# Kernel optimization log

Hardware: AMD Instinct MI355X
Metric: run time of the kernel (lower is better)

Reference implementation:

```python
import jax, jax.numpy as jnp
import numpy as np

B, T, C, E, H, K = 4, 2048, 1024, 8, 2048, 2


def setup_inputs() -> dict:
    key = jax.random.key(0)
    k1, k2, k3, k4 = jax.random.split(key, 4)
    x = jax.random.normal(k1, (B, T, C), jnp.float32)
    router_w = jax.random.normal(k2, (E, C), jnp.float32) * 0.02
    fc_w = jax.random.normal(k3, (E, H, C), jnp.float32) * 0.02
    proj_w = jax.random.normal(k4, (E, C, H), jnp.float32) * 0.02
    return {"x": x, "router_w": router_w, "fc_w": fc_w, "proj_w": proj_w}


def reference(x, router_w, fc_w, proj_w):
    Bb, Tt, Cc = x.shape
    Ee = router_w.shape[0]
    k = K
    N = Bb * Tt
    x_flat = x.reshape(N, Cc)

    # Router: linear -> softmax -> top-k, renormalize
    scores = x_flat @ router_w.T                       # [N, E]
    routing_weights = jax.nn.softmax(scores, axis=-1)  # [N, E]
    top_w, top_idx = jax.lax.top_k(routing_weights, k) # [N, k]
    top_w = top_w / (top_w.sum(-1, keepdims=True) + 1e-10)

    flat_expert_ids = top_idx.reshape(-1)              # [N*k]
    flat_weights = top_w.reshape(-1)
    flat_token_ids = jnp.repeat(jnp.arange(N), k)

    # Stable sort by expert id (token permute)
    order = jnp.argsort(flat_expert_ids, stable=True)
    se = flat_expert_ids[order]
    st = flat_token_ids[order]
    sw = flat_weights[order]
    permuted_x = x_flat[st]                            # [N*k, C]

    tokens_per_expert = jnp.bincount(flat_expert_ids, length=Ee)
    offsets = jnp.concatenate([jnp.zeros((1,), tokens_per_expert.dtype),
                               jnp.cumsum(tokens_per_expert)[:-1]])
    pos_in_expert = jnp.arange(N * k) - offsets[se]
    capacity = 2 * N * k // Ee
    flat_batch_idx = se * capacity + pos_in_expert
    valid = pos_in_expert < capacity

    # Scatter tokens into capacity-padded per-expert batches (overflow dropped)
    scatter_idx = jnp.where(valid, flat_batch_idx, Ee * capacity)  # OOB => drop
    batched_x = jnp.zeros((Ee * capacity, Cc), x.dtype).at[scatter_idx].set(
        permuted_x, mode='drop')
    batched_x = batched_x.reshape(Ee, capacity, Cc)

    # Grouped GEMM: fc -> relu^2 -> proj
    hidden = jnp.square(jax.nn.relu(jnp.einsum('eic,ehc->eih', batched_x, fc_w)))
    batched_out = jnp.einsum('eih,ech->eic', hidden, proj_w).reshape(Ee * capacity, Cc)

    # Gather back, weight, scatter-add combine
    gathered = batched_out[jnp.where(valid, flat_batch_idx, 0)]
    weighted = gathered * jnp.where(valid, sw, 0.0)[:, None]
    output = jnp.zeros((N, Cc), x.dtype).at[st].add(weighted)
    return output.reshape(Bb, Tt, Cc), routing_weights.reshape(Bb, Tt, Ee)
```

## Files before the change

### kernel.cpp

```cpp
#include <hip/hip_runtime.h>
#include <hip/hip_bf16.h>
#include <stdint.h>

#define NB 4
#define NTT 2048
#define NC 1024
#define NE 8
#define NH 2048
#define NKK 2
#define NTOK (NB * NTT)
#define CAP (2 * NTOK * NKK / NE)

typedef __hip_bfloat16 bf16;
typedef __attribute__((ext_vector_type(8))) short short8;
typedef __attribute__((ext_vector_type(4))) short short4v;
typedef __attribute__((ext_vector_type(4))) float floatx4;
typedef __attribute__((ext_vector_type(2))) float floatx2;

typedef const __attribute__((address_space(1))) void* gas_ptr;
typedef __attribute__((address_space(3))) void* las_ptr;

static __device__ __forceinline__ void async_copy16(const void* g, void* l) {
  __builtin_amdgcn_global_load_lds((gas_ptr)g, (las_ptr)l, 16, 0, 0);
}

static __device__ __forceinline__ unsigned short f2b(float f) {
  bf16 h = __float2bfloat16(f);
  unsigned short u;
  __builtin_memcpy(&u, &h, 2);
  return u;
}
static __device__ __forceinline__ int iclamp(int v, int lo, int hi) {
  return v < lo ? lo : (v > hi ? hi : v);
}

__global__ __launch_bounds__(256) void zero_out_kernel(float* __restrict__ out) {
  const size_t i = ((size_t)blockIdx.x * 256 + threadIdx.x) * 4;
  floatx4 z = {0.f, 0.f, 0.f, 0.f};
  *reinterpret_cast<floatx4*>(out + i) = z;
}

__global__ __launch_bounds__(256) void cvt_kernel(const float* __restrict__ src,
                                                  bf16* __restrict__ dst) {
  const size_t i = ((size_t)blockIdx.x * 256 + threadIdx.x) * 8;
  const floatx4 a = *reinterpret_cast<const floatx4*>(src + i);
  const floatx4 b = *reinterpret_cast<const floatx4*>(src + i + 4);
  short8 r;
  r[0] = (short)f2b(a[0]); r[1] = (short)f2b(a[1]);
  r[2] = (short)f2b(a[2]); r[3] = (short)f2b(a[3]);
  r[4] = (short)f2b(b[0]); r[5] = (short)f2b(b[1]);
  r[6] = (short)f2b(b[2]); r[7] = (short)f2b(b[3]);
  *reinterpret_cast<short8*>(dst + i) = r;
}

__global__ __launch_bounds__(256) void router_kernel(
    const float* __restrict__ x, const float* __restrict__ rw,
    float* __restrict__ rw_out, int* __restrict__ epair,
    float* __restrict__ wpair, bf16* __restrict__ xb) {
  __shared__ float rws[NE * NC];
  const int tid = threadIdx.x;
  {
    const floatx4* rw4 = reinterpret_cast<const floatx4*>(rw);
    floatx4* rwl4 = reinterpret_cast<floatx4*>(rws);
#pragma unroll
    for (int i = 0; i < 8; ++i) rwl4[i * 256 + tid] = rw4[i * 256 + tid];
  }
  __syncthreads();

  const int wave = tid >> 6;
  const int lane = tid & 63;
  const int t = blockIdx.x * 4 + wave;
  const floatx4* xr4 = reinterpret_cast<const floatx4*>(x + (size_t)t * NC);
  const floatx4* rwl4 = reinterpret_cast<const floatx4*>(rws);
  bf16* xbr = xb + (size_t)t * NC;

  floatx4 xv[4];
#pragma unroll
  for (int i = 0; i < 4; ++i) xv[i] = xr4[i * 64 + lane];

#pragma unroll
  for (int i = 0; i < 4; ++i) {
    const int idx = i * 64 + lane;
    short4v o;
    o[0] = (short)f2b(xv[i][0]); o[1] = (short)f2b(xv[i][1]);
    o[2] = (short)f2b(xv[i][2]); o[3] = (short)f2b(xv[i][3]);
    *reinterpret_cast<short4v*>(xbr + idx * 4) = o;
  }

  float acc[NE];
#pragma unroll
  for (int e = 0; e < NE; ++e) acc[e] = 0.f;
#pragma unroll
  for (int i = 0; i < 4; ++i) {
    const int idx = i * 64 + lane;
#pragma unroll
    for (int e = 0; e < NE; ++e) {
      const floatx4 wv = rwl4[e * 256 + idx];
      acc[e] = fmaf(xv[i][0], wv[0], acc[e]);
      acc[e] = fmaf(xv[i][1], wv[1], acc[e]);
      acc[e] = fmaf(xv[i][2], wv[2], acc[e]);
      acc[e] = fmaf(xv[i][3], wv[3], acc[e]);
    }
  }
#pragma unroll
  for (int e = 0; e < NE; ++e) {
#pragma unroll
    for (int off = 32; off; off >>= 1) acc[e] += __shfl_xor(acc[e], off, 64);
  }

  float m = acc[0];
#pragma unroll
  for (int e = 1; e < NE; ++e) m = fmaxf(m, acc[e]);
  float p[NE];
  float s = 0.f;
#pragma unroll
  for (int e = 0; e < NE; ++e) {
    p[e] = __expf(acc[e] - m);
    s += p[e];
  }
  const float inv = 1.f / s;
#pragma unroll
  for (int e = 0; e < NE; ++e) p[e] *= inv;

  if (lane < NE) rw_out[(size_t)t * NE + lane] = p[lane];

  if (lane == 0) {
    int i0 = 0;
    float v0 = p[0];
    int i1 = -1;
    float v1 = -1.f;
#pragma unroll
    for (int e = 1; e < NE; ++e) {
      if (p[e] > v0) {
        v1 = v0; i1 = i0;
        v0 = p[e]; i0 = e;
      } else if (p[e] > v1) {
        v1 = p[e]; i1 = e;
      }
    }
    i0 = iclamp(i0, 0, NE - 1);
    i1 = iclamp(i1, 0, NE - 1);
    const float denom = v0 + v1 + 1e-10f;
    epair[t] = i0 | (i1 << 16);
    floatx2 wv;
    wv[0] = v0 / denom;
    wv[1] = v1 / denom;
    *reinterpret_cast<floatx2*>(wpair + 2 * t) = wv;
  }
}

__global__ __launch_bounds__(256) void build_kernel(
    const int* __restrict__ epair, const float* __restrict__ wpair,
    int* __restrict__ cnt, int* __restrict__ tok, float* __restrict__ wslot) {
  const int e = blockIdx.x;
  const int tid = threadIdx.x;
  const int lane = tid & 63;
  const int wave = tid >> 6;
  constexpr int TPT = NTOK / 256;
  const int t0 = tid * TPT;

  int pe[TPT];
#pragma unroll
  for (int i = 0; i < TPT; i += 4) {
    const int4 v = *reinterpret_cast<const int4*>(epair + t0 + i);
    pe[i] = v.x; pe[i + 1] = v.y; pe[i + 2] = v.z; pe[i + 3] = v.w;
  }
  int c = 0;
#pragma unroll
  for (int i = 0; i < TPT; ++i)
    c += (((pe[i] & 0xffff) == e) ? 1 : 0) + (((pe[i] >> 16) == e) ? 1 : 0);

  int incl = c;
#pragma unroll
  for (int off = 1; off < 64; off <<= 1) {
    const int up = __shfl_up(incl, off, 64);
    if (lane >= off) incl += up;
  }
  __shared__ int wsum[4];
  if (lane == 63) wsum[wave] = incl;
  __syncthreads();
  int base = incl - c;
#pragma unroll
  for (int w = 0; w < 4; ++w)
    if (w < wave) base += wsum[w];
  if (tid == 255) cnt[e] = base + c;

#pragma unroll
  for (int i = 0; i < TPT; ++i) {
    const int t = t0 + i;
    if ((pe[i] & 0xffff) == e) {
      if (base < CAP) {
        tok[e * CAP + base] = t;
        wslot[e * CAP + base] = wpair[2 * t];
      }
      ++base;
    }
    if ((pe[i] >> 16) == e) {
      if (base < CAP) {
        tok[e * CAP + base] = t;
        wslot[e * CAP + base] = wpair[2 * t + 1];
      }
      ++base;
    }
  }
}

template <bool FC>
__global__ __launch_bounds__(256) void gemm_moe(
    const bf16* __restrict__ Axb, const bf16* __restrict__ Ah,
    const bf16* __restrict__ Bw, bf16* __restrict__ Oh,
    float* __restrict__ Oo, const int* __restrict__ cnt,
    const int* __restrict__ tok, const float* __restrict__ wslot,
    int rowOffset, int mch) {
  constexpr int Kd = FC ? NC : NH;
  constexpr int Nd = FC ? NH : NC;
  const int e = blockIdx.z;
  const int Me = iclamp(cnt[e], 0, CAP);
  const int rowBase = rowOffset + blockIdx.y * 128;
  if (rowBase >= Me) return;
  const int colBase = blockIdx.x * 128;

  const bf16* __restrict__ Be = Bw + (size_t)e * Nd * Kd;
  const bf16* __restrict__ Ahc = Ah + (size_t)e * mch * NH;

  __shared__ bf16 As[128 * 64];
  __shared__ bf16 Bs[128 * 64];

  const int tid = threadIdx.x;
  const int lane = tid & 63;
  const int wid = tid >> 6;
  const int wm = wid & 1;
  const int wn = wid >> 1;
  const int ml = lane & 15;
  const int quad = lane >> 4;

  const bf16* ga[4];
  const bf16* gb[4];
  bf16* la[4];
  bf16* lb[4];
#pragma unroll
  for (int it = 0; it < 4; ++it) {
    const int sidx = it * 256 + tid;
    const int r = sidx >> 3;
    const int pc = sidx & 7;
    const int lc = pc ^ (r & 7);
    if (FC) {
      const int grow = rowBase + r;
      const int tk = (grow < Me) ? tok[e * CAP + grow] : 0;
      const int arow = iclamp(tk, 0, NTOK - 1);
      ga[it] = Axb + (size_t)arow * NC + lc * 8;
    } else {
      int grow = rowBase + r;
      if (grow > Me - 1) grow = Me - 1;
      const int arow = iclamp(grow - rowOffset, 0, mch - 1);
      ga[it] = Ahc + (size_t)arow * NH + lc * 8;
    }
    gb[it] = Be + (size_t)(colBase + r) * Kd + lc * 8;
    la[it] = As + sidx * 8;
    lb[it] = Bs + sidx * 8;
  }

  floatx4 acc[4][4];
#pragma unroll
  for (int mt = 0; mt < 4; ++mt)
#pragma unroll
    for (int nt = 0; nt < 4; ++nt) acc[mt][nt] = floatx4{0.f, 0.f, 0.f, 0.f};

  int aoff[4][2], boff[4][2];
#pragma unroll
  for (int t4 = 0; t4 < 4; ++t4)
#pragma unroll
    for (int kk = 0; kk < 2; ++kk) {
      const int ra = wm * 64 + t4 * 16 + ml;
      const int rb = wn * 64 + t4 * 16 + ml;
      const int q = kk * 4 + quad;
      aoff[t4][kk] = (ra * 8 + (q ^ (ra & 7))) * 8;
      boff[t4][kk] = (rb * 8 + (q ^ (rb & 7))) * 8;
    }

#pragma unroll
  for (int it = 0; it < 4; ++it) async_copy16(ga[it], la[it]);
#pragma unroll
  for (int it = 0; it < 4; ++it) async_copy16(gb[it], lb[it]);

  const int nkb = Kd >> 6;
  for (int kb = 0; kb < nkb; ++kb) {
    __syncthreads();
    short8 af[4][2], bff[4][2];
#pragma unroll
    for (int mt = 0; mt < 4; ++mt)
#pragma unroll
      for (int kk = 0; kk < 2; ++kk)
        af[mt][kk] = *reinterpret_cast<const short8*>(&As[aoff[mt][kk]]);
#pragma unroll
    for (int nt = 0; nt < 4; ++nt)
#pragma unroll
      for (int kk = 0; kk < 2; ++kk)
        bff[nt][kk] = *reinterpret_cast<const short8*>(&Bs[boff[nt][kk]]);
#pragma unroll
    for (int kk = 0; kk < 2; ++kk)
#pragma unroll
      for (int mt = 0; mt < 4; ++mt)
#pragma unroll
        for (int nt = 0; nt < 4; ++nt)
          acc[mt][nt] = __builtin_amdgcn_mfma_f32_16x16x32_bf16(
              af[mt][kk], bff[nt][kk], acc[mt][nt], 0, 0, 0);
    __syncthreads();
    if (kb + 1 < nkb) {
      const int k0 = (kb + 1) << 6;
#pragma unroll
      for (int it = 0; it < 4; ++it) async_copy16(ga[it] + k0, la[it]);
#pragma unroll
      for (int it = 0; it < 4; ++it) async_copy16(gb[it] + k0, lb[it]);
    }
  }

  if (FC) {
    bf16* __restrict__ O = Oh + (size_t)e * mch * NH;
    const int rlBase = rowBase - rowOffset;
#pragma unroll
    for (int mt = 0; mt < 4; ++mt) {
      const int rl = wm * 64 + mt * 16 + quad * 4;
#pragma unroll
      for (int nt = 0; nt < 4; ++nt) {
        const int cc = colBase + wn * 64 + nt * 16 + ml;
        const floatx4 v = acc[mt][nt];
#pragma unroll
        for (int rg = 0; rg < 4; ++rg) {
          if (rowBase + rl + rg < Me) {
            float f = fmaxf(v[rg], 0.f);
            f = f * f;
            O[(size_t)(rlBase + rl + rg) * NH + cc] = __float2bfloat16(f);
          }
        }
      }
    }
  } else {
#pragma unroll
    for (int mt = 0; mt < 4; ++mt) {
      const int rl = wm * 64 + mt * 16 + quad * 4;
#pragma unroll
      for (int rg = 0; rg < 4; ++rg) {
        const int re = rowBase + rl + rg;
        if (re < Me) {
          const int t = iclamp(tok[e * CAP + re], 0, NTOK - 1);
          const float w = wslot[e * CAP + re];
#pragma unroll
          for (int nt = 0; nt < 4; ++nt) {
            const int cc = colBase + wn * 64 + nt * 16 + ml;
            atomicAdd(Oo + (size_t)t * NC + cc, w * acc[mt][nt][rg]);
          }
        }
      }
    }
  }
}

extern "C" void kernel_launch(void* const* d_in, const int* in_sizes, int n_in,
                              void* d_out, int out_size, void* d_ws,
                              size_t ws_size, hipStream_t stream) {
  const float* x = (const float*)d_in[0];
  const float* rw = (const float*)d_in[1];
  const float* fcw = (const float*)d_in[2];
  const float* pjw = (const float*)d_in[3];
  float* out = (float*)d_out;
  float* rw_out = out + (size_t)NTOK * NC;

  char* ws = (char*)d_ws;
  int* cnt = (int*)ws;
  int* tok = (int*)(ws + 256);
  float* wslot = (float*)(ws + 256 + 131072);
  int* epair = (int*)(ws + 262400);
  float* wpair = (float*)(ws + 262400 + 32768);
  bf16* xb = (bf16*)(ws + 360704);
  bf16* fcwb = (bf16*)(ws + 360704 + 16777216);
  bf16* pjwb = (bf16*)(ws + 360704 + 16777216 + 33554432);
  const size_t fixed = 360704 + 16777216 + 2 * 33554432;
  bf16* hidden = (bf16*)(ws + fixed);
  (void)in_sizes; (void)n_in; (void)out_size;

  int mch = 128;
  for (int cand = CAP; cand >= 128; cand >>= 1) {
    const size_t need = fixed + (size_t)NE * cand * NH * 2;
    if (need <= ws_size) { mch = cand; break; }
  }

  zero_out_kernel<<<NTOK * NC / 1024, 256, 0, stream>>>(out);
  cvt_kernel<<<NE * NH * NC / 2048, 256, 0, stream>>>(fcw, fcwb);
  cvt_kernel<<<NE * NC * NH / 2048, 256, 0, stream>>>(pjw, pjwb);
  router_kernel<<<NTOK / 4, 256, 0, stream>>>(x, rw, rw_out, epair, wpair, xb);
  build_kernel<<<NE, 256, 0, stream>>>(epair, wpair, cnt, tok, wslot);

  for (int c = 0; c < CAP / mch; ++c) {
    gemm_moe<true><<<dim3(NH / 128, mch / 128, NE), 256, 0, stream>>>(
        xb, hidden, fcwb, hidden, out, cnt, tok, wslot, c * mch, mch);
    gemm_moe<false><<<dim3(NC / 128, mch / 128, NE), 256, 0, stream>>>(
        xb, hidden, pjwb, hidden, out, cnt, tok, wslot, c * mch, mch);
  }
}
```

Measured before the change: 475.0 us.

## Use 256x256 tiles, 512 threads and double-buffered LDS pipeline in MoE GEMM

The grouped GEMM block tile grows from 128x128 to 256x256 with 512 threads and 8x4 MFMA tiles per wave. The K loop becomes a double-buffered LDS pipeline: the next slice is prefetched with explicit vmcnt waits and raw barriers, and MFMA sections get raised priority. The aim is more operand reuse per load and global-to-LDS copies hidden behind compute. In exchange LDS use rises to 128 KB per block and register pressure is higher, which may limit occupancy. Partially filled expert tiles also waste more work because tile granularity is coarser.

```diff
diff --git a/kernel.cpp b/kernel.cpp
--- a/kernel.cpp
+++ b/kernel.cpp
@@ -206,7 +206,7 @@
 }
 
 template <bool FC>
-__global__ __launch_bounds__(256) void gemm_moe(
+__global__ __launch_bounds__(512, 2) void gemm_moe(
     const bf16* __restrict__ Axb, const bf16* __restrict__ Ah,
     const bf16* __restrict__ Bw, bf16* __restrict__ Oh,
     float* __restrict__ Oo, const int* __restrict__ cnt,
@@ -216,15 +216,15 @@
   constexpr int Nd = FC ? NH : NC;
   const int e = blockIdx.z;
   const int Me = iclamp(cnt[e], 0, CAP);
-  const int rowBase = rowOffset + blockIdx.y * 128;
+  const int rowBase = rowOffset + blockIdx.y * 256;
   if (rowBase >= Me) return;
-  const int colBase = blockIdx.x * 128;
+  const int colBase = blockIdx.x * 256;
 
   const bf16* __restrict__ Be = Bw + (size_t)e * Nd * Kd;
   const bf16* __restrict__ Ahc = Ah + (size_t)e * mch * NH;
 
-  __shared__ bf16 As[128 * 64];
-  __shared__ bf16 Bs[128 * 64];
+  __shared__ bf16 As[2][256 * 64];
+  __shared__ bf16 Bs[2][256 * 64];
 
   const int tid = threadIdx.x;
   const int lane = tid & 63;
@@ -236,11 +236,10 @@
 
   const bf16* ga[4];
   const bf16* gb[4];
-  bf16* la[4];
-  bf16* lb[4];
+  int lofs[4];
 #pragma unroll
   for (int it = 0; it < 4; ++it) {
-    const int sidx = it * 256 + tid;
+    const int sidx = it * 512 + tid;
     const int r = sidx >> 3;
     const int pc = sidx & 7;
     const int lc = pc ^ (r & 7);
@@ -256,71 +255,80 @@
       ga[it] = Ahc + (size_t)arow * NH + lc * 8;
     }
     gb[it] = Be + (size_t)(colBase + r) * Kd + lc * 8;
-    la[it] = As + sidx * 8;
-    lb[it] = Bs + sidx * 8;
-  }
-
-  floatx4 acc[4][4];
-#pragma unroll
-  for (int mt = 0; mt < 4; ++mt)
+    lofs[it] = sidx * 8;
+  }
+
+  floatx4 acc[8][4];
+#pragma unroll
+  for (int mt = 0; mt < 8; ++mt)
 #pragma unroll
     for (int nt = 0; nt < 4; ++nt) acc[mt][nt] = floatx4{0.f, 0.f, 0.f, 0.f};
 
-  int aoff[4][2], boff[4][2];
-#pragma unroll
-  for (int t4 = 0; t4 < 4; ++t4)
+  int aoff[8], boff[4];
+#pragma unroll
+  for (int mt = 0; mt < 8; ++mt) {
+    const int ra = wm * 128 + mt * 16 + ml;
+    aoff[mt] = (ra * 8 + (quad ^ (ra & 7))) * 8;
+  }
+#pragma unroll
+  for (int nt = 0; nt < 4; ++nt) {
+    const int rb = wn * 64 + nt * 16 + ml;
+    boff[nt] = (rb * 8 + (quad ^ (rb & 7))) * 8;
+  }
+
+#pragma unroll
+  for (int it = 0; it < 4; ++it) async_copy16(ga[it], &As[0][lofs[it]]);
+#pragma unroll
+  for (int it = 0; it < 4; ++it) async_copy16(gb[it], &Bs[0][lofs[it]]);
+
+  const int nkb = Kd >> 6;
+  for (int t = 0; t < nkb; ++t) {
+    const int b = t & 1;
+    if (t + 1 < nkb) {
+      const int k0 = (t + 1) << 6;
+#pragma unroll
+      for (int it = 0; it < 4; ++it)
+        async_copy16(ga[it] + k0, &As[b ^ 1][lofs[it]]);
+#pragma unroll
+      for (int it = 0; it < 4; ++it)
+        async_copy16(gb[it] + k0, &Bs[b ^ 1][lofs[it]]);
+      asm volatile("s_waitcnt vmcnt(8)" ::: "memory");
+    } else {
+      asm volatile("s_waitcnt vmcnt(0)" ::: "memory");
+    }
+    __builtin_amdgcn_s_barrier();
+    __builtin_amdgcn_sched_barrier(0);
 #pragma unroll
     for (int kk = 0; kk < 2; ++kk) {
-      const int ra = wm * 64 + t4 * 16 + ml;
-      const int rb = wn * 64 + t4 * 16 + ml;
-      const int q = kk * 4 + quad;
-      aoff[t4][kk] = (ra * 8 + (q ^ (ra & 7))) * 8;
-      boff[t4][kk] = (rb * 8 + (q ^ (rb & 7))) * 8;
-    }
-
-#pragma unroll
-  for (int it = 0; it < 4; ++it) async_copy16(ga[it], la[it]);
-#pragma unroll
-  for (int it = 0; it < 4; ++it) async_copy16(gb[it], lb[it]);
-
-  const int nkb = Kd >> 6;
-  for (int kb = 0; kb < nkb; ++kb) {
-    __syncthreads();
-    short8 af[4][2], bff[4][2];
-#pragma unroll
-    for (int mt = 0; mt < 4; ++mt)
-#pragma unroll
-      for (int kk = 0; kk < 2; ++kk)
-        af[mt][kk] = *reinterpret_cast<const short8*>(&As[aoff[mt][kk]]);
-#pragma unroll
-    for (int nt = 0; nt < 4; ++nt)
-#pragma unroll
-      for (int kk = 0; kk < 2; ++kk)
-        bff[nt][kk] = *reinterpret_cast<const short8*>(&Bs[boff[nt][kk]]);
-#pragma unroll
-    for (int kk = 0; kk < 2; ++kk)
-#pragma unroll
-      for (int mt = 0; mt < 4; ++mt)
+      const int x = kk * 32;
+      short8 af[8], bf[4];
+#pragma unroll
+      for (int mt = 0; mt < 8; ++mt)
+        af[mt] = *reinterpret_cast<const short8*>(&As[b][aoff[mt] ^ x]);
+#pragma unroll
+      for (int nt = 0; nt < 4; ++nt)
+        bf[nt] = *reinterpret_cast<const short8*>(&Bs[b][boff[nt] ^ x]);
+      asm volatile("s_waitcnt lgkmcnt(0)" ::: "memory");
+      __builtin_amdgcn_sched_barrier(0);
+      __builtin_amdgcn_s_setprio(1);
+#pragma unroll
+      for (int mt = 0; mt < 8; ++mt)
 #pragma unroll
         for (int nt = 0; nt < 4; ++nt)
           acc[mt][nt] = __builtin_amdgcn_mfma_f32_16x16x32_bf16(
-              af[mt][kk], bff[nt][kk], acc[mt][nt], 0, 0, 0);
-    __syncthreads();
-    if (kb + 1 < nkb) {
-      const int k0 = (kb + 1) << 6;
-#pragma unroll
-      for (int it = 0; it < 4; ++it) async_copy16(ga[it] + k0, la[it]);
-#pragma unroll
-      for (int it = 0; it < 4; ++it) async_copy16(gb[it] + k0, lb[it]);
-    }
+              af[mt], bf[nt], acc[mt][nt], 0, 0, 0);
+      __builtin_amdgcn_s_setprio(0);
+    }
+    __builtin_amdgcn_s_barrier();
+    __builtin_amdgcn_sched_barrier(0);
   }
 
   if (FC) {
     bf16* __restrict__ O = Oh + (size_t)e * mch * NH;
     const int rlBase = rowBase - rowOffset;
 #pragma unroll
-    for (int mt = 0; mt < 4; ++mt) {
-      const int rl = wm * 64 + mt * 16 + quad * 4;
+    for (int mt = 0; mt < 8; ++mt) {
+      const int rl = wm * 128 + mt * 16 + quad * 4;
 #pragma unroll
       for (int nt = 0; nt < 4; ++nt) {
         const int cc = colBase + wn * 64 + nt * 16 + ml;
@@ -337,8 +345,8 @@
     }
   } else {
 #pragma unroll
-    for (int mt = 0; mt < 4; ++mt) {
-      const int rl = wm * 64 + mt * 16 + quad * 4;
+    for (int mt = 0; mt < 8; ++mt) {
+      const int rl = wm * 128 + mt * 16 + quad * 4;
 #pragma unroll
       for (int rg = 0; rg < 4; ++rg) {
         const int re = rowBase + rl + rg;
@@ -379,8 +387,8 @@
   bf16* hidden = (bf16*)(ws + fixed);
   (void)in_sizes; (void)n_in; (void)out_size;
 
-  int mch = 128;
-  for (int cand = CAP; cand >= 128; cand >>= 1) {
+  int mch = 256;
+  for (int cand = CAP; cand >= 256; cand >>= 1) {
     const size_t need = fixed + (size_t)NE * cand * NH * 2;
     if (need <= ws_size) { mch = cand; break; }
   }
@@ -392,9 +400,9 @@
   build_kernel<<<NE, 256, 0, stream>>>(epair, wpair, cnt, tok, wslot);
 
   for (int c = 0; c < CAP / mch; ++c) {
-    gemm_moe<true><<<dim3(NH / 128, mch / 128, NE), 256, 0, stream>>>(
+    gemm_moe<true><<<dim3(NH / 256, mch / 256, NE), 512, 0, stream>>>(
         xb, hidden, fcwb, hidden, out, cnt, tok, wslot, c * mch, mch);
-    gemm_moe<false><<<dim3(NC / 128, mch / 128, NE), 256, 0, stream>>>(
+    gemm_moe<false><<<dim3(NC / 256, mch / 256, NE), 512, 0, stream>>>(
         xb, hidden, pjwb, hidden, out, cnt, tok, wslot, c * mch, mch);
   }
 }
```

After: 486.5 us. 2.4% more time.
